# Kernel tuning notes

Measured on AMD Instinct MI355X. Metric: run time of the kernel, lower is better.

## Reference

```python
import jax, jax.numpy as jnp
import numpy as np

B, H, Q, D = 8, 16, 256, 128
BLOCK_SIZE = 16
MAX_BLOCKS = 256          # blocks per sequence -> kv_len = 4096
NUM_BLOCKS = B * MAX_BLOCKS  # physical pool = 2048 blocks
NEG_INF = -1e9


def setup_inputs() -> dict:
    key = jax.random.key(0)
    k1, k2, k3, k4, k5 = jax.random.split(key, 5)
    q = jax.random.normal(k1, (B, H, Q, D), dtype=jnp.float32)
    k_cache = jax.random.normal(k2, (NUM_BLOCKS, H, BLOCK_SIZE, D), dtype=jnp.float32)
    v_cache = jax.random.normal(k3, (NUM_BLOCKS, H, BLOCK_SIZE, D), dtype=jnp.float32)
    # each sequence owns a disjoint, shuffled set of physical blocks (realistic paging)
    perm = jax.random.permutation(k4, NUM_BLOCKS)
    block_tables = perm.reshape(B, MAX_BLOCKS).astype(jnp.int32)
    # valid lengths in [2048, 4096] so softmax rows are never fully masked
    seq_lens = jax.random.randint(k5, (B,), 2048, MAX_BLOCKS * BLOCK_SIZE + 1).astype(jnp.int32)
    return {"q": q, "k_cache": k_cache, "v_cache": v_cache,
            "block_tables": block_tables, "seq_lens": seq_lens}


def paged_attention(q, k_cache, v_cache, block_tables, seq_lens):
    # Gather physical KV blocks per sequence via block tables.
    # k_cache: [N_blocks, H, bs, D]; block_tables: [B, M]
    k = k_cache[block_tables]                       # [B, M, H, bs, D]
    v = v_cache[block_tables]                       # [B, M, H, bs, D]
    kv_len = k.shape[1] * k.shape[3]
    k = jnp.transpose(k, (0, 2, 1, 3, 4)).reshape(q.shape[0], q.shape[1], kv_len, q.shape[3])
    v = jnp.transpose(v, (0, 2, 1, 3, 4)).reshape(q.shape[0], q.shape[1], kv_len, q.shape[3])
    scale = 1.0 / jnp.sqrt(jnp.asarray(q.shape[-1], q.dtype))
    scores = jnp.einsum('bhqd,bhkd->bhqk', q, k) * scale  # [B,H,Q,KV]
    pos = jnp.arange(kv_len)
    valid = pos[None, :] < seq_lens[:, None]               # [B, KV]
    scores = jnp.where(valid[:, None, None, :], scores, NEG_INF)
    attn = jax.nn.softmax(scores, axis=-1)
    return jnp.einsum('bhqk,bhkd->bhqd', attn, v)          # [B,H,Q,D]


def reference(q, k_cache, v_cache, block_tables, seq_lens):
    return paged_attention(q, k_cache, v_cache, block_tables, seq_lens)
```

## Files before the change

kernel.cpp:

```cpp
#include <hip/hip_runtime.h>
#include <hip/hip_bf16.h>

#define BB     8
#define HH     16
#define QLEN   256
#define DH     128
#define BSZ    16
#define MAXB   256
#define KT     64
#define BHQ    (BB*HH*QLEN)
#define VROW   144

typedef __attribute__((ext_vector_type(8)))  short bf16x8;
typedef __attribute__((ext_vector_type(16))) float f32x16;
typedef __attribute__((ext_vector_type(2)))  unsigned uint2v;

__device__ __forceinline__ unsigned pk2(float a, float b) {
  union { __hip_bfloat162 h; unsigned u; } c;
  c.h = __float22bfloat162_rn(make_float2(a, b));
  return c.u;
}

__device__ __forceinline__ float bf2f(unsigned short u) {
  union { float f; unsigned u; } c; c.u = ((unsigned)u) << 16; return c.f;
}

__device__ __forceinline__ float fexp2(float x) {
#if __has_builtin(__builtin_amdgcn_exp2f)
  return __builtin_amdgcn_exp2f(x);
#else
  return exp2f(x);
#endif
}

__device__ __forceinline__ uint2v swap_halves(unsigned a, unsigned b, int hi) {
#if __has_builtin(__builtin_amdgcn_permlane32_swap)
  (void)hi;
  return __builtin_amdgcn_permlane32_swap(a, b, false, false);
#else
  const unsigned pa  = (unsigned)__shfl_xor((int)a, 32);
  const unsigned pb_ = (unsigned)__shfl_xor((int)b, 32);
  uint2v r;
  r[0] = hi ? pb_ : a;
  r[1] = hi ? b : pa;
  return r;
#endif
}

__device__ __forceinline__ f32x16 mfma32(bf16x8 a, bf16x8 b, f32x16 c) {
  return __builtin_amdgcn_mfma_f32_32x32x16_bf16(a, b, c, 0, 0, 0);
}

#define BARRIER_KEEP_LOADS() \
  asm volatile("s_waitcnt lgkmcnt(0)\n\ts_barrier" ::: "memory")

__launch_bounds__(512, 2)
__global__ void paged_attn_kernel(const float* __restrict__ qg,
                                  const float* __restrict__ kc,
                                  const float* __restrict__ vc,
                                  const int* __restrict__ bt,
                                  const int* __restrict__ sl,
                                  float* __restrict__ outd,
                                  __hip_bfloat16* __restrict__ opart,
                                  float* __restrict__ lpart,
                                  int nkv) {
  __shared__ __align__(16) char kls[2][16 * 1024];
  __shared__ __align__(16) char vls[2][DH * VROW];
  __shared__ int btab[MAXB];

  const int tid  = threadIdx.x;
  const int wave = tid >> 6;
  const int lane = tid & 63;
  const int ll   = lane & 31;
  const int hi   = lane >> 5;

  const int bid = blockIdx.x;
  const int c   = bid % nkv;
  const int bh  = bid / nkv;
  const int b   = bh >> 4;
  const int h   = bh & 15;

  const int seq = sl[b];
  const int nt  = (seq + KT - 1) / KT;
  const int per = (nt + nkv - 1) / nkv;
  const int t0  = c * per;
  const int t1  = (t0 + per < nt) ? (t0 + per) : nt;

  if (tid < MAXB) btab[tid] = bt[b * MAXB + tid];
  __syncthreads();

  const int krb   = tid >> 4;
  const int kc16  = tid & 15;
  const int kcbase = h * (BSZ * DH) + (krb & 15) * DH + kc16 * 8;
  const int d4  = tid & 31;
  const int kvq = tid >> 5;
  const int vcbase = h * (BSZ * DH) + ((kvq & 3) * 4) * DH + d4 * 4;

  float4 kreg[2][2];
  float4 vreg[4];

#define ISSUE_LOADS(KV0)                                                        \
  {                                                                             \
    const int tb = (KV0) >> 4;                                                  \
    _Pragma("unroll")                                                           \
    for (int i = 0; i < 2; ++i) {                                               \
      const int phys = btab[tb + i * 2 + (krb >> 4)];                           \
      const float* kp = kc + (((size_t)phys) << 15) + kcbase;                   \
      kreg[i][0] = *(const float4*)(kp);                                        \
      kreg[i][1] = *(const float4*)(kp + 4);                                    \
    }                                                                           \
    {                                                                           \
      const int phys = btab[tb + (kvq >> 2)];                                   \
      const float* vp = vc + (((size_t)phys) << 15) + vcbase;                   \
      vreg[0] = *(const float4*)(vp);                                           \
      vreg[1] = *(const float4*)(vp + DH);                                      \
      vreg[2] = *(const float4*)(vp + 2 * DH);                                  \
      vreg[3] = *(const float4*)(vp + 3 * DH);                                  \
    }                                                                           \
  }

#define STAGE_WRITE(BUF)                                                        \
  {                                                                             \
    _Pragma("unroll")                                                           \
    for (int i = 0; i < 2; ++i) {                                               \
      const int row = i * 32 + krb;                                             \
      union { uint4 u4; unsigned u[4]; } w;                                     \
      w.u[0] = pk2(kreg[i][0].x, kreg[i][0].y);                                 \
      w.u[1] = pk2(kreg[i][0].z, kreg[i][0].w);                                 \
      w.u[2] = pk2(kreg[i][1].x, kreg[i][1].y);                                 \
      w.u[3] = pk2(kreg[i][1].z, kreg[i][1].w);                                 \
      *(uint4*)(kls[BUF] + kc16 * 1024 + ((row ^ (kc16 & 7)) << 4)) = w.u4;     \
    }                                                                           \
    {                                                                           \
      const float* v0 = (const float*)&vreg[0];                                 \
      const float* v1 = (const float*)&vreg[1];                                 \
      const float* v2 = (const float*)&vreg[2];                                 \
      const float* v3 = (const float*)&vreg[3];                                 \
      _Pragma("unroll")                                                         \
      for (int jj = 0; jj < 4; ++jj) {                                          \
        const int d  = d4 * 4 + jj;                                             \
        const int vb = d * VROW + ((kvq * 8) ^ (((d >> 3) & 7) << 4));          \
        *(uint2*)(vls[BUF] + vb) =                                              \
            make_uint2(pk2(v0[jj], v1[jj]), pk2(v2[jj], v3[jj]));               \
      }                                                                         \
    }                                                                           \
  }

  ISSUE_LOADS(t0 * KT)

  const float qscale = 0.08838834764831845f * 1.4426950408889634f;
  const int qbase = wave * 32;
  bf16x8 qf[8];
  {
    const float* qr = qg + ((size_t)bh * QLEN + qbase + ll) * DH;
#pragma unroll
    for (int ks = 0; ks < 8; ++ks) {
      const int d0 = ks * 16 + hi * 8;
      const float4 a  = *(const float4*)(qr + d0);
      const float4 bv = *(const float4*)(qr + d0 + 4);
      union { bf16x8 v; unsigned u[4]; } w;
      w.u[0] = pk2(a.x * qscale,  a.y * qscale);
      w.u[1] = pk2(a.z * qscale,  a.w * qscale);
      w.u[2] = pk2(bv.x * qscale, bv.y * qscale);
      w.u[3] = pk2(bv.z * qscale, bv.w * qscale);
      qf[ks] = w.v;
    }
  }

  f32x16 accT[4];
#pragma unroll
  for (int dt = 0; dt < 4; ++dt)
#pragma unroll
    for (int i = 0; i < 16; ++i) accT[dt][i] = 0.f;
  float lrow = 0.f;

  STAGE_WRITE(t0 & 1)
  if (t0 + 1 < t1) ISSUE_LOADS((t0 + 1) * KT)
  BARRIER_KEEP_LOADS();

  for (int t = t0; t < t1; ++t) {
    const int kv0 = t * KT;
    const int bb  = t & 1;

    f32x16 s[2];
#pragma unroll
    for (int i = 0; i < 16; ++i) { s[0][i] = -16.f; s[1][i] = -16.f; }
#pragma unroll
    for (int ks = 0; ks < 8; ++ks) {
      const int cch = 2 * ks + hi;
      const char* cb = kls[bb] + cch * 1024;
      const bf16x8 kf0 = *(const bf16x8*)(cb + (((ll)      ^ (cch & 7)) << 4));
      const bf16x8 kf1 = *(const bf16x8*)(cb + (((32 + ll) ^ (cch & 7)) << 4));
      s[0] = mfma32(kf0, qf[ks], s[0]);
      s[1] = mfma32(kf1, qf[ks], s[1]);
    }

    if (t + 1 < t1) STAGE_WRITE(bb ^ 1)
    if (t + 2 < t1) ISSUE_LOADS((t + 2) * KT)

    if (kv0 + KT > seq) {
#pragma unroll
      for (int kvt = 0; kvt < 2; ++kvt)
#pragma unroll
        for (int r = 0; r < 16; ++r) {
          const int kvg = kv0 + kvt * 32 + (r & 3) + 8 * (r >> 2) + 4 * hi;
          if (kvg >= seq) s[kvt][r] = -1e30f;
        }
    }
#pragma unroll
    for (int kvt = 0; kvt < 2; ++kvt)
#pragma unroll
      for (int r = 0; r < 16; ++r)
        s[kvt][r] = fexp2(s[kvt][r]);
    float ts[16];
#pragma unroll
    for (int r = 0; r < 16; ++r) ts[r] = s[0][r] + s[1][r];
#pragma unroll
    for (int w2 = 8; w2 >= 1; w2 >>= 1)
#pragma unroll
      for (int r = 0; r < w2; ++r) ts[r] += ts[r + w2];
    {
      union { float f; unsigned u; } cu; cu.f = ts[0];
      const uint2v sr = swap_halves(cu.u, cu.u, hi);
      union { unsigned u; float f; } a0, a1; a0.u = sr[0]; a1.u = sr[1];
      lrow += a0.f + a1.f;
    }

    unsigned pkk[2][8];
#pragma unroll
    for (int kvt = 0; kvt < 2; ++kvt)
#pragma unroll
      for (int p = 0; p < 8; ++p)
        pkk[kvt][p] = pk2(s[kvt][2 * p], s[kvt][2 * p + 1]);

    bf16x8 pb[4];
#pragma unroll
    for (int kvb = 0; kvb < 4; ++kvb) {
      const int kvt = kvb >> 1;
      const int base = (kvb & 1) * 4;
      const uint2v e0 = swap_halves(pkk[kvt][base],     pkk[kvt][base + 2], hi);
      const uint2v e1 = swap_halves(pkk[kvt][base + 1], pkk[kvt][base + 3], hi);
      union { bf16x8 v; unsigned u[4]; } w;
      w.u[0] = e0[0]; w.u[1] = e1[0]; w.u[2] = e0[1]; w.u[3] = e1[1];
      pb[kvb] = w.v;
    }

#pragma unroll
    for (int dt = 0; dt < 4; ++dt) {
      const int d  = dt * 32 + ll;
      const int sw = ((d >> 3) & 7) << 4;
      const char* vbp = vls[bb] + d * VROW;
#pragma unroll
      for (int kvb = 0; kvb < 4; ++kvb) {
        const bf16x8 va = *(const bf16x8*)(vbp + ((kvb * 32 + hi * 16) ^ sw));
        accT[dt] = mfma32(va, pb[kvb], accT[dt]);
      }
    }

    BARRIER_KEEP_LOADS();
  }

  const int grow = bh * QLEN + qbase + ll;
  if (nkv == 1) {
    const float inv = 1.0f / lrow;
    float* orow = outd + (size_t)grow * DH;
#pragma unroll
    for (int dt = 0; dt < 4; ++dt)
#pragma unroll
      for (int r = 0; r < 4; ++r) {
        float4 v = make_float4(accT[dt][4 * r] * inv,     accT[dt][4 * r + 1] * inv,
                               accT[dt][4 * r + 2] * inv, accT[dt][4 * r + 3] * inv);
        *(float4*)(orow + dt * 32 + 8 * r + 4 * hi) = v;
      }
  } else {
    __hip_bfloat16* orow = opart + ((size_t)c * BHQ + grow) * DH;
#pragma unroll
    for (int dt = 0; dt < 4; ++dt)
#pragma unroll
      for (int r = 0; r < 4; ++r) {
        const unsigned lo2 = pk2(accT[dt][4 * r],     accT[dt][4 * r + 1]);
        const unsigned hi2 = pk2(accT[dt][4 * r + 2], accT[dt][4 * r + 3]);
        *(uint2*)((char*)orow + (dt * 32 + 8 * r + 4 * hi) * 2) = make_uint2(lo2, hi2);
      }
    if (hi == 0) lpart[c * BHQ + grow] = lrow;
  }
}

__global__ void combine_kernel(const __hip_bfloat16* __restrict__ op,
                               const float* __restrict__ lp,
                               float* __restrict__ out, int nkv) {
  const int idx = blockIdx.x * 256 + threadIdx.x;
  const int row = idx >> 4;
  float den = 0.f;
  float o[8] = {0.f, 0.f, 0.f, 0.f, 0.f, 0.f, 0.f, 0.f};
  for (int cc = 0; cc < nkv; ++cc) {
    den += lp[cc * BHQ + row];
    const uint4 v = *(const uint4*)((const char*)op + ((size_t)cc * BHQ * DH + (size_t)idx * 8) * 2);
    const unsigned u[4] = {v.x, v.y, v.z, v.w};
#pragma unroll
    for (int j = 0; j < 4; ++j) {
      o[2 * j]     += bf2f((unsigned short)(u[j] & 0xffffu));
      o[2 * j + 1] += bf2f((unsigned short)(u[j] >> 16));
    }
  }
  const float inv = 1.0f / den;
  float4* dst = (float4*)(out + (size_t)idx * 8);
  dst[0] = make_float4(o[0] * inv, o[1] * inv, o[2] * inv, o[3] * inv);
  dst[1] = make_float4(o[4] * inv, o[5] * inv, o[6] * inv, o[7] * inv);
}

extern "C" void kernel_launch(void* const* d_in, const int* in_sizes, int n_in,
                              void* d_out, int out_size, void* d_ws, size_t ws_size,
                              hipStream_t stream) {
  const float* q  = (const float*)d_in[0];
  const float* kc = (const float*)d_in[1];
  const float* vc = (const float*)d_in[2];
  const int* bt   = (const int*)d_in[3];
  const int* sl   = (const int*)d_in[4];
  float* out = (float*)d_out;

  const size_t perchunk = (size_t)BHQ * DH * sizeof(__hip_bfloat16) + (size_t)BHQ * sizeof(float);
  int nkv = 1;
  if (ws_size >= 4 * perchunk) nkv = 4;
  else if (ws_size >= 2 * perchunk) nkv = 2;

  __hip_bfloat16* op = (__hip_bfloat16*)d_ws;
  float* lp = (float*)((char*)d_ws + (size_t)nkv * BHQ * DH * sizeof(__hip_bfloat16));

  paged_attn_kernel<<<dim3(BB * HH * nkv), dim3(512), 0, stream>>>(q, kc, vc, bt, sl, out, op, lp, nkv);
  if (nkv > 1)
    combine_kernel<<<dim3(BHQ * DH / 8 / 256), dim3(256), 0, stream>>>(op, lp, out, nkv);
}
```

Baseline: 116.3 us.

## Balance split-KV work across sequences by proportional slot allocation

Replaces the fixed per-sequence KV split (nkv chunks per batch-head) with a global pool of 32 slots per head. The slots are divided among sequences in proportion to their tile counts using largest-remainder rounding. Each workgroup and the combine kernel recompute the same quota table from seq_lens to find their sequence and tile range. This is meant to even out load when sequence lengths vary, at the cost of per-thread quota computation and more combine bookkeeping.

After: 164.2 us. 41.2% more time.

```diff
diff --git a/kernel.cpp b/kernel.cpp
--- a/kernel.cpp
+++ b/kernel.cpp
@@ -10,6 +10,7 @@
 #define KT     64
 #define BHQ    (BB*HH*QLEN)
 #define VROW   144
+#define NSLOT  32
 
 typedef __attribute__((ext_vector_type(8)))  short bf16x8;
 typedef __attribute__((ext_vector_type(16))) float f32x16;
@@ -54,6 +55,28 @@
 #define BARRIER_KEEP_LOADS() \
   asm volatile("s_waitcnt lgkmcnt(0)\n\ts_barrier" ::: "memory")
 
+struct Quota { int q[BB]; int P[BB + 1]; int per[BB]; int nt[BB]; };
+__device__ __forceinline__ void quotas(const int* __restrict__ sl, Quota& Q) {
+  int T = 0;
+  for (int b = 0; b < BB; ++b) { Q.nt[b] = (sl[b] + KT - 1) / KT; T += Q.nt[b]; }
+  int rem[BB], sum = 0;
+  for (int b = 0; b < BB; ++b) {
+    const int f = Q.nt[b] * NSLOT;
+    Q.q[b] = f / T; rem[b] = f % T; sum += Q.q[b];
+  }
+  for (int e = sum; e < NSLOT; ++e) {
+    int best = 0, bestrem = -1;
+    for (int b = 0; b < BB; ++b)
+      if (rem[b] > bestrem) { bestrem = rem[b]; best = b; }
+    Q.q[best] += 1; rem[best] = -1;
+  }
+  Q.P[0] = 0;
+  for (int b = 0; b < BB; ++b) {
+    Q.P[b + 1] = Q.P[b] + Q.q[b];
+    Q.per[b] = (Q.nt[b] + Q.q[b] - 1) / Q.q[b];
+  }
+}
+
 __launch_bounds__(512, 2)
 __global__ void paged_attn_kernel(const float* __restrict__ qg,
                                   const float* __restrict__ kc,
@@ -63,7 +86,7 @@
                                   float* __restrict__ outd,
                                   __hip_bfloat16* __restrict__ opart,
                                   float* __restrict__ lpart,
-                                  int nkv) {
+                                  int bal) {
   __shared__ __align__(16) char kls[2][16 * 1024];
   __shared__ __align__(16) char vls[2][DH * VROW];
   __shared__ int btab[MAXB];
@@ -75,16 +98,24 @@
   const int hi   = lane >> 5;
 
   const int bid = blockIdx.x;
-  const int c   = bid % nkv;
-  const int bh  = bid / nkv;
-  const int b   = bh >> 4;
-  const int h   = bh & 15;
-
-  const int seq = sl[b];
-  const int nt  = (seq + KT - 1) / KT;
-  const int per = (nt + nkv - 1) / nkv;
-  const int t0  = c * per;
-  const int t1  = (t0 + per < nt) ? (t0 + per) : nt;
+  const int NW  = bal ? NSLOT : BB;
+  const int h   = bid / NW;
+  const int w   = bid % NW;
+
+  int b, t0, t1;
+  if (bal) {
+    Quota Q; quotas(sl, Q);
+    b = 0;
+    while (w >= Q.P[b + 1]) ++b;
+    const int c = w - Q.P[b];
+    t0 = c * Q.per[b];
+    const int te = t0 + Q.per[b];
+    t1 = te < Q.nt[b] ? te : Q.nt[b];
+    if (t0 >= t1) return;
+  } else {
+    b = w; t0 = 0; t1 = (sl[b] + KT - 1) / KT;
+  }
+  const int bh = b * HH + h;
 
   if (tid < MAXB) btab[tid] = bt[b * MAXB + tid];
   __syncthreads();
@@ -124,12 +155,12 @@
     _Pragma("unroll")                                                           \
     for (int i = 0; i < 2; ++i) {                                               \
       const int row = i * 32 + krb;                                             \
-      union { uint4 u4; unsigned u[4]; } w;                                     \
-      w.u[0] = pk2(kreg[i][0].x, kreg[i][0].y);                                 \
-      w.u[1] = pk2(kreg[i][0].z, kreg[i][0].w);                                 \
-      w.u[2] = pk2(kreg[i][1].x, kreg[i][1].y);                                 \
-      w.u[3] = pk2(kreg[i][1].z, kreg[i][1].w);                                 \
-      *(uint4*)(kls[BUF] + kc16 * 1024 + ((row ^ (kc16 & 7)) << 4)) = w.u4;     \
+      union { uint4 u4; unsigned u[4]; } w_;                                    \
+      w_.u[0] = pk2(kreg[i][0].x, kreg[i][0].y);                                \
+      w_.u[1] = pk2(kreg[i][0].z, kreg[i][0].w);                                \
+      w_.u[2] = pk2(kreg[i][1].x, kreg[i][1].y);                                \
+      w_.u[3] = pk2(kreg[i][1].z, kreg[i][1].w);                                \
+      *(uint4*)(kls[BUF] + kc16 * 1024 + ((row ^ (kc16 & 7)) << 4)) = w_.u4;    \
     }                                                                           \
     {                                                                           \
       const float* v0 = (const float*)&vreg[0];                                 \
@@ -158,12 +189,12 @@
       const int d0 = ks * 16 + hi * 8;
       const float4 a  = *(const float4*)(qr + d0);
       const float4 bv = *(const float4*)(qr + d0 + 4);
-      union { bf16x8 v; unsigned u[4]; } w;
-      w.u[0] = pk2(a.x * qscale,  a.y * qscale);
-      w.u[1] = pk2(a.z * qscale,  a.w * qscale);
-      w.u[2] = pk2(bv.x * qscale, bv.y * qscale);
-      w.u[3] = pk2(bv.z * qscale, bv.w * qscale);
-      qf[ks] = w.v;
+      union { bf16x8 v; unsigned u[4]; } w_;
+      w_.u[0] = pk2(a.x * qscale,  a.y * qscale);
+      w_.u[1] = pk2(a.z * qscale,  a.w * qscale);
+      w_.u[2] = pk2(bv.x * qscale, bv.y * qscale);
+      w_.u[3] = pk2(bv.z * qscale, bv.w * qscale);
+      qf[ks] = w_.v;
     }
   }
 
@@ -178,6 +209,7 @@
   if (t0 + 1 < t1) ISSUE_LOADS((t0 + 1) * KT)
   BARRIER_KEEP_LOADS();
 
+  const int seq = sl[b];
   for (int t = t0; t < t1; ++t) {
     const int kv0 = t * KT;
     const int bb  = t & 1;
@@ -240,9 +272,9 @@
       const int base = (kvb & 1) * 4;
       const uint2v e0 = swap_halves(pkk[kvt][base],     pkk[kvt][base + 2], hi);
       const uint2v e1 = swap_halves(pkk[kvt][base + 1], pkk[kvt][base + 3], hi);
-      union { bf16x8 v; unsigned u[4]; } w;
-      w.u[0] = e0[0]; w.u[1] = e1[0]; w.u[2] = e0[1]; w.u[3] = e1[1];
-      pb[kvb] = w.v;
+      union { bf16x8 v; unsigned u[4]; } w_;
+      w_.u[0] = e0[0]; w_.u[1] = e1[0]; w_.u[2] = e0[1]; w_.u[3] = e1[1];
+      pb[kvb] = w_.v;
     }
 
 #pragma unroll
@@ -260,10 +292,9 @@
     BARRIER_KEEP_LOADS();
   }
 
-  const int grow = bh * QLEN + qbase + ll;
-  if (nkv == 1) {
+  if (!bal) {
     const float inv = 1.0f / lrow;
-    float* orow = outd + (size_t)grow * DH;
+    float* orow = outd + ((size_t)bh * QLEN + qbase + ll) * DH;
 #pragma unroll
     for (int dt = 0; dt < 4; ++dt)
 #pragma unroll
@@ -273,7 +304,7 @@
         *(float4*)(orow + dt * 32 + 8 * r + 4 * hi) = v;
       }
   } else {
-    __hip_bfloat16* orow = opart + ((size_t)c * BHQ + grow) * DH;
+    __hip_bfloat16* orow = opart + ((size_t)bid * QLEN + qbase + ll) * DH;
 #pragma unroll
     for (int dt = 0; dt < 4; ++dt)
 #pragma unroll
@@ -282,20 +313,32 @@
         const unsigned hi2 = pk2(accT[dt][4 * r + 2], accT[dt][4 * r + 3]);
         *(uint2*)((char*)orow + (dt * 32 + 8 * r + 4 * hi) * 2) = make_uint2(lo2, hi2);
       }
-    if (hi == 0) lpart[c * BHQ + grow] = lrow;
+    if (hi == 0) lpart[bid * QLEN + qbase + ll] = lrow;
   }
 }
 
 __global__ void combine_kernel(const __hip_bfloat16* __restrict__ op,
                                const float* __restrict__ lp,
-                               float* __restrict__ out, int nkv) {
+                               const int* __restrict__ sl,
+                               float* __restrict__ out) {
   const int idx = blockIdx.x * 256 + threadIdx.x;
   const int row = idx >> 4;
+  const int g8  = idx & 15;
+  const int q   = row & (QLEN - 1);
+  const int bh  = row >> 8;
+  const int b   = bh >> 4;
+  const int h   = bh & 15;
+
+  Quota Q; quotas(sl, Q);
+
   float den = 0.f;
   float o[8] = {0.f, 0.f, 0.f, 0.f, 0.f, 0.f, 0.f, 0.f};
-  for (int cc = 0; cc < nkv; ++cc) {
-    den += lp[cc * BHQ + row];
-    const uint4 v = *(const uint4*)((const char*)op + ((size_t)cc * BHQ * DH + (size_t)idx * 8) * 2);
+  for (int c = 0; c < Q.q[b]; ++c) {
+    if (c * Q.per[b] >= Q.nt[b]) break;
+    const int slot = h * NSLOT + Q.P[b] + c;
+    den += lp[slot * QLEN + q];
+    const uint4 v = *(const uint4*)((const char*)op +
+                    (((size_t)slot * QLEN + q) * DH + g8 * 8) * 2);
     const unsigned u[4] = {v.x, v.y, v.z, v.w};
 #pragma unroll
     for (int j = 0; j < 4; ++j) {
@@ -304,7 +347,7 @@
     }
   }
   const float inv = 1.0f / den;
-  float4* dst = (float4*)(out + (size_t)idx * 8);
+  float4* dst = (float4*)(out + (size_t)row * DH + g8 * 8);
   dst[0] = make_float4(o[0] * inv, o[1] * inv, o[2] * inv, o[3] * inv);
   dst[1] = make_float4(o[4] * inv, o[5] * inv, o[6] * inv, o[7] * inv);
 }
@@ -319,15 +362,16 @@
   const int* sl   = (const int*)d_in[4];
   float* out = (float*)d_out;
 
-  const size_t perchunk = (size_t)BHQ * DH * sizeof(__hip_bfloat16) + (size_t)BHQ * sizeof(float);
-  int nkv = 1;
-  if (ws_size >= 4 * perchunk) nkv = 4;
-  else if (ws_size >= 2 * perchunk) nkv = 2;
+  const int G = HH * NSLOT;
+  const size_t need = (size_t)G * QLEN * DH * sizeof(__hip_bfloat16)
+                    + (size_t)G * QLEN * sizeof(float);
+  const int bal = (ws_size >= need) ? 1 : 0;
 
   __hip_bfloat16* op = (__hip_bfloat16*)d_ws;
-  float* lp = (float*)((char*)d_ws + (size_t)nkv * BHQ * DH * sizeof(__hip_bfloat16));
-
-  paged_attn_kernel<<<dim3(BB * HH * nkv), dim3(512), 0, stream>>>(q, kc, vc, bt, sl, out, op, lp, nkv);
-  if (nkv > 1)
-    combine_kernel<<<dim3(BHQ * DH / 8 / 256), dim3(256), 0, stream>>>(op, lp, out, nkv);
-}
+  float* lp = (float*)((char*)d_ws + (size_t)G * QLEN * DH * sizeof(__hip_bfloat16));
+
+  const int grid = bal ? G : (HH * BB);
+  paged_attn_kernel<<<dim3(grid), dim3(512), 0, stream>>>(q, kc, vc, bt, sl, out, op, lp, bal);
+  if (bal)
+    combine_kernel<<<dim3(BHQ * DH / 8 / 256), dim3(256), 0, stream>>>(op, lp, sl, out);
+}
```
